# Kernel tuning notes

Measured on AMD Instinct MI355X. Metric: run time of the kernel, lower is better.

The kernel has to match this reference:

```python
import jax, jax.numpy as jnp
import numpy as np

N, E, B, D, H, C = 50000, 800000, 128, 64, 128, 2
EPS = 1e-5


def setup_inputs() -> dict:
    key = jax.random.key(0)
    ks = jax.random.split(key, 12)
    s = 0.1
    return {
        "x": jax.random.normal(ks[0], (N, D), jnp.float32),
        "edge_index": jax.random.randint(ks[1], (2, E), 0, N, jnp.int64),
        "batch": jnp.sort(jax.random.randint(ks[2], (N,), 0, B, jnp.int64)),
        "W_l": jax.random.normal(ks[3], (D, D), jnp.float32) * s,
        "b_l": jnp.zeros((D,), jnp.float32),
        "W_r": jax.random.normal(ks[4], (D, D), jnp.float32) * s,
        "W_res": jax.random.normal(ks[5], (D, D), jnp.float32) * s,
        "b_res": jnp.zeros((D,), jnp.float32),
        "gamma": jnp.ones((D,), jnp.float32),
        "beta": jnp.zeros((D,), jnp.float32),
        "gate_W1": jax.random.normal(ks[6], (D, D), jnp.float32) * s,
        "gate_b1": jnp.zeros((D,), jnp.float32),
        "gate_W2": jax.random.normal(ks[7], (D, 1), jnp.float32) * s,
        "gate_b2": jnp.zeros((1,), jnp.float32),
        "W_p1": jax.random.normal(ks[8], (D, H), jnp.float32) * s,
        "b_p1": jnp.zeros((H,), jnp.float32),
        "W_p2": jax.random.normal(ks[9], (H, C), jnp.float32) * s,
        "b_p2": jnp.zeros((C,), jnp.float32),
    }


def reference(x, edge_index, batch, W_l, b_l, W_r, W_res, b_res, gamma, beta,
              gate_W1, gate_b1, gate_W2, gate_b2, W_p1, b_p1, W_p2, b_p2):
    src, dst = edge_index[0], edge_index[1]
    # SAGEConv, mean aggregation: gather source feats, scatter-mean to target
    agg = jax.ops.segment_sum(x[src], dst, num_segments=N)          # [N, D]
    cnt = jax.ops.segment_sum(jnp.ones((E,), x.dtype), dst, num_segments=N)
    mean = agg / jnp.maximum(cnt, 1.0)[:, None]
    h = mean @ W_l + b_l + x @ W_r                                   # [N, D]
    # dropout is identity (eval mode)
    # BatchNorm1d (training-mode math: biased batch stats)
    mu = jnp.mean(h, axis=0)
    var = jnp.var(h, axis=0)
    h = (h - mu) * jax.lax.rsqrt(var + EPS) * gamma + beta
    # residual projection of the original features
    h = h + x @ W_res + b_res
    # GlobalAttention pooling: per-graph softmax over gate scores
    gate = jax.nn.relu(h @ gate_W1 + gate_b1) @ gate_W2 + gate_b2    # [N, 1]
    g = gate[:, 0]
    gmax = jax.ops.segment_max(g, batch, num_segments=B)
    gmax = jnp.where(jnp.isfinite(gmax), gmax, 0.0)
    e = jnp.exp(g - gmax[batch])
    z = jax.ops.segment_sum(e, batch, num_segments=B)
    alpha = e / jnp.maximum(z, 1e-16)[batch]
    pooled = jax.ops.segment_sum(alpha[:, None] * h, batch, num_segments=B)  # [B, D]
    # 2-layer predictor MLP with ReLU between
    out = jax.nn.relu(pooled @ W_p1 + b_p1) @ W_p2 + b_p2            # [B, C]
    return out
```

## Files before the change

kernel.cpp:

```cpp
#include <hip/hip_runtime.h>
#include <math.h>

#define N_NODES 50000
#define N_EDGES 800000
#define BATCHES 128
#define DIM 64
#define HID 128
#define NCLS 2
#define EPSV 1e-5f
#define MAXD 64

#define NPART 8
#define PART_SZ ((N_NODES + NPART - 1) / NPART)
#define EPB 2048
#define NCHK_E ((N_EDGES + EPB - 1) / EPB)
#define NCHUNK1 782

typedef __attribute__((ext_vector_type(8))) short bf16x8;
typedef __attribute__((ext_vector_type(4))) float f32x4;

__device__ __forceinline__ unsigned short f2bf(float f){
  unsigned u = __float_as_uint(f);
  u += 0x7FFFu + ((u >> 16) & 1u);
  return (unsigned short)(u >> 16);
}
__device__ __forceinline__ float bf2f(unsigned short h){
  return __uint_as_float(((unsigned)h) << 16);
}
__device__ __forceinline__ void split2(float f, unsigned short& hi, unsigned short& lo){
  hi = f2bf(f);
  lo = f2bf(f - bf2f(hi));
}
__device__ __forceinline__ uint4 pack8(const unsigned short* s){
  uint4 u;
  u.x = (unsigned)s[0] | ((unsigned)s[1] << 16);
  u.y = (unsigned)s[2] | ((unsigned)s[3] << 16);
  u.z = (unsigned)s[4] | ((unsigned)s[5] << 16);
  u.w = (unsigned)s[6] | ((unsigned)s[7] << 16);
  return u;
}

__global__ void k_scatter(const int* __restrict__ ei, int* __restrict__ cnt,
                          unsigned short* __restrict__ csr){
  const int p = blockIdx.x & (NPART-1);
  const int c = blockIdx.x >> 3;
  const int lo = p * PART_SZ;
  const int hi = lo + PART_SZ;
  const int e0 = c * EPB;
  const int e1 = (e0 + EPB < N_EDGES) ? e0 + EPB : N_EDGES;
  for (int i = e0 + threadIdx.x; i < e1; i += 256){
    int d = ei[N_EDGES + i];
    if (d >= lo && d < hi){
      int s = ei[i];
      int pos = atomicAdd(&cnt[d], 1);
      csr[(size_t)d*MAXD + pos] = (unsigned short)s;
    }
  }
}

__global__ void __launch_bounds__(256) k_lin1(
    const float* __restrict__ x, const unsigned short* __restrict__ csr,
    const int* __restrict__ cnt,
    const float* __restrict__ Wl, const float* __restrict__ bl,
    const float* __restrict__ Wr, float* __restrict__ hbuf,
    float* __restrict__ pstat){
  __shared__ __align__(16) short sB[2][64][136];
  __shared__ __align__(16) short sA[2][64][72];
  const int tid  = threadIdx.x;
  const int lane = tid & 63, w = tid >> 6;
  const int g    = lane >> 4, f = lane & 15;
  const int jc   = lane & 15;
  const int mrow = 16*w + jc;
  const int koff = (lane >> 4) * 8;
  const int r0   = 16*w + (lane >> 4)*4;
  const int base = blockIdx.x * 64;

  {
    const int k0 = 32 * w;
    #pragma unroll
    for (int kc = 0; kc < 4; ++kc){
      unsigned short h[8], l[8];
      #pragma unroll
      for (int i = 0; i < 8; ++i){
        int k = k0 + 8*kc + i;
        float v = (k < 64) ? Wl[k*DIM + lane] : Wr[(k-64)*DIM + lane];
        split2(v, h[i], l[i]);
      }
      *(uint4*)&sB[0][lane][k0 + 8*kc] = pack8(h);
      *(uint4*)&sB[1][lane][k0 + 8*kc] = pack8(l);
    }
  }
  __syncthreads();

  float blv[4];
  #pragma unroll
  for (int nt = 0; nt < 4; ++nt) blv[nt] = bl[nt*16 + jc];

  f32x4 acc[4] = {};
  #pragma unroll
  for (int half = 0; half < 2; ++half){
    if (half == 0){
      for (int n = 0; n < 16; ++n){
        const int node = base + 16*w + n;
        int dg = 0;
        if (node < N_NODES) dg = cnt[node];
        const size_t start = (size_t)node * MAXD;
        int e = (lane < dg) ? (int)csr[start + lane] : 0;
        float4 a4 = make_float4(0.f,0.f,0.f,0.f);
        int i = 0;
        for (; i + 16 <= dg; i += 16){
          int s0 = __shfl(e, i +      g, 64);
          int s1 = __shfl(e, i + 4  + g, 64);
          int s2 = __shfl(e, i + 8  + g, 64);
          int s3 = __shfl(e, i + 12 + g, 64);
          float4 v0 = *(const float4*)&x[(size_t)s0*DIM + f*4];
          float4 v1 = *(const float4*)&x[(size_t)s1*DIM + f*4];
          float4 v2 = *(const float4*)&x[(size_t)s2*DIM + f*4];
          float4 v3 = *(const float4*)&x[(size_t)s3*DIM + f*4];
          a4.x += v0.x + v1.x + v2.x + v3.x;
          a4.y += v0.y + v1.y + v2.y + v3.y;
          a4.z += v0.z + v1.z + v2.z + v3.z;
          a4.w += v0.w + v1.w + v2.w + v3.w;
        }
        for (; i < dg; i += 4){
          int idx = i + g;
          int srcl = (idx < dg) ? idx : (dg - 1);
          int s = __shfl(e, srcl, 64);
          if (idx < dg){
            float4 v = *(const float4*)&x[(size_t)s*DIM + f*4];
            a4.x += v.x; a4.y += v.y; a4.z += v.z; a4.w += v.w;
          }
        }
        a4.x += __shfl_xor(a4.x, 16, 64); a4.x += __shfl_xor(a4.x, 32, 64);
        a4.y += __shfl_xor(a4.y, 16, 64); a4.y += __shfl_xor(a4.y, 32, 64);
        a4.z += __shfl_xor(a4.z, 16, 64); a4.z += __shfl_xor(a4.z, 32, 64);
        a4.w += __shfl_xor(a4.w, 16, 64); a4.w += __shfl_xor(a4.w, 32, 64);
        if (g == 0){
          float inv = 1.f / fmaxf((float)dg, 1.f);
          unsigned short h[4], l[4];
          split2(a4.x*inv,h[0],l[0]); split2(a4.y*inv,h[1],l[1]);
          split2(a4.z*inv,h[2],l[2]); split2(a4.w*inv,h[3],l[3]);
          uint2 ph, pl;
          ph.x = (unsigned)h[0] | ((unsigned)h[1]<<16);
          ph.y = (unsigned)h[2] | ((unsigned)h[3]<<16);
          pl.x = (unsigned)l[0] | ((unsigned)l[1]<<16);
          pl.y = (unsigned)l[2] | ((unsigned)l[3]<<16);
          *(uint2*)&sA[0][16*w + n][f*4] = ph;
          *(uint2*)&sA[1][16*w + n][f*4] = pl;
        }
      }
    } else {
      #pragma unroll
      for (int s4 = 0; s4 < 4; ++s4){
        const int row = 16*w + s4*4 + g;
        const int node = base + row;
        float4 v = make_float4(0.f,0.f,0.f,0.f);
        if (node < N_NODES) v = *(const float4*)&x[(size_t)node*DIM + f*4];
        unsigned short h[4], l[4];
        split2(v.x,h[0],l[0]); split2(v.y,h[1],l[1]);
        split2(v.z,h[2],l[2]); split2(v.w,h[3],l[3]);
        uint2 ph, pl;
        ph.x = (unsigned)h[0] | ((unsigned)h[1]<<16);
        ph.y = (unsigned)h[2] | ((unsigned)h[3]<<16);
        pl.x = (unsigned)l[0] | ((unsigned)l[1]<<16);
        pl.y = (unsigned)l[2] | ((unsigned)l[3]<<16);
        *(uint2*)&sA[0][row][f*4] = ph;
        *(uint2*)&sA[1][row][f*4] = pl;
      }
    }
    #pragma unroll
    for (int kt2 = 0; kt2 < 2; ++kt2){
      const int ka = kt2*32 + koff;
      const int kb = half*64 + ka;
      bf16x8 ah = *(const bf16x8*)&sA[0][mrow][ka];
      bf16x8 al = *(const bf16x8*)&sA[1][mrow][ka];
      #pragma unroll
      for (int nt = 0; nt < 4; ++nt){
        const int nr = nt*16 + jc;
        bf16x8 bh = *(const bf16x8*)&sB[0][nr][kb];
        bf16x8 bo = *(const bf16x8*)&sB[1][nr][kb];
        acc[nt] = __builtin_amdgcn_mfma_f32_16x16x32_bf16(ah, bh, acc[nt], 0,0,0);
        acc[nt] = __builtin_amdgcn_mfma_f32_16x16x32_bf16(al, bh, acc[nt], 0,0,0);
        acc[nt] = __builtin_amdgcn_mfma_f32_16x16x32_bf16(ah, bo, acc[nt], 0,0,0);
      }
    }
  }

  float s1[4] = {0.f,0.f,0.f,0.f}, s2[4] = {0.f,0.f,0.f,0.f};
  #pragma unroll
  for (int nt = 0; nt < 4; ++nt){
    const int col = nt*16 + jc;
    #pragma unroll
    for (int r = 0; r < 4; ++r){
      const int node = base + r0 + r;
      float v = acc[nt][r] + blv[nt];
      if (node < N_NODES){
        hbuf[(size_t)node*DIM + col] = v;
        s1[nt] += v; s2[nt] += v*v;
      }
    }
  }

  __syncthreads();
  float* sred = (float*)sA;
  #pragma unroll
  for (int nt = 0; nt < 4; ++nt){
    float a = s1[nt], b = s2[nt];
    a += __shfl_xor(a, 16, 64); a += __shfl_xor(a, 32, 64);
    b += __shfl_xor(b, 16, 64); b += __shfl_xor(b, 32, 64);
    if ((lane >> 4) == 0){
      sred[0*256 + w*64 + nt*16 + jc] = a;
      sred[1*256 + w*64 + nt*16 + jc] = b;
    }
  }
  __syncthreads();
  if (tid < 64){
    float a = sred[tid] + sred[64+tid] + sred[128+tid] + sred[192+tid];
    float b = sred[256+tid] + sred[320+tid] + sred[384+tid] + sred[448+tid];
    pstat[(size_t)blockIdx.x*128 + tid]      = a;
    pstat[(size_t)blockIdx.x*128 + 64 + tid] = b;
  }
}

__global__ void __launch_bounds__(256) k_stats(
    const float* __restrict__ pstat, float* __restrict__ muinv){
  __shared__ float r1[256], r2[256];
  const int j = blockIdx.x;
  const int t = threadIdx.x;
  float s1 = 0.f, s2 = 0.f;
  for (int c = t; c < NCHUNK1; c += 256){
    s1 += pstat[(size_t)c*128 + j];
    s2 += pstat[(size_t)c*128 + 64 + j];
  }
  r1[t] = s1; r2[t] = s2;
  __syncthreads();
  for (int st = 128; st > 0; st >>= 1){
    if (t < st){ r1[t] += r1[t+st]; r2[t] += r2[t+st]; }
    __syncthreads();
  }
  if (t == 0){
    float mu = r1[0] / (float)N_NODES;
    float var = r2[0] / (float)N_NODES - mu*mu;
    muinv[j] = mu;
    muinv[DIM+j] = 1.0f / sqrtf(var + EPSV);
  }
}

__device__ __forceinline__ void stage_w64(short* sWh, short* sWl_,
                                          const float* __restrict__ W,
                                          int w, int lane){
  const int k0 = 16 * w;
  #pragma unroll
  for (int kc = 0; kc < 2; ++kc){
    unsigned short h[8], l[8];
    #pragma unroll
    for (int i = 0; i < 8; ++i){
      int k = k0 + 8*kc + i;
      split2(W[k*DIM + lane], h[i], l[i]);
    }
    *(uint4*)&sWh[lane*72 + k0 + 8*kc] = pack8(h);
    *(uint4*)&sWl_[lane*72 + k0 + 8*kc] = pack8(l);
  }
}

__global__ void __launch_bounds__(256) k_lin2(
    const float* __restrict__ x, const float* __restrict__ hbuf,
    const float* __restrict__ Wres, const float* __restrict__ bres,
    const float* __restrict__ gamma, const float* __restrict__ beta,
    const float* __restrict__ muinv,
    const float* __restrict__ gW1, const float* __restrict__ gb1,
    const float* __restrict__ gW2, const float* __restrict__ gb2,
    const int* __restrict__ batch,
    float* __restrict__ zbuf, float* __restrict__ pooled){
  __shared__ __align__(16) short sW[2][64][72];
  __shared__ __align__(16) short sA[2][64][72];
  __shared__ int sb[64];
  __shared__ unsigned long long runmask;
  const int tid  = threadIdx.x;
  const int lane = tid & 63, w = tid >> 6;
  const int jc   = lane & 15;
  const int g16  = w*4 + (lane >> 4);
  const int mrow = 16*w + jc;
  const int koff = (lane >> 4) * 8;
  const int r0   = 16*w + (lane >> 4)*4;
  const int base = blockIdx.x * 64;

  float muv[4], invv[4], gav[4], bev[4], brv[4], g1v[4], w2v[4];
  #pragma unroll
  for (int nt = 0; nt < 4; ++nt){
    const int col = nt*16 + jc;
    muv[nt] = muinv[col];  invv[nt] = muinv[DIM+col];
    gav[nt] = gamma[col];  bev[nt]  = beta[col];
    brv[nt] = bres[col];   g1v[nt]  = gb1[col];
    w2v[nt] = gW2[col];
  }
  const float gb2v = gb2[0];

  {
    const int row = tid >> 2;
    const int kq  = (tid & 3) * 16;
    const int node = base + row;
    #pragma unroll
    for (int cc = 0; cc < 4; ++cc){
      float4 v = make_float4(0.f,0.f,0.f,0.f);
      if (node < N_NODES) v = *(const float4*)&x[(size_t)node*DIM + kq + 4*cc];
      unsigned short h[4], l[4];
      split2(v.x,h[0],l[0]); split2(v.y,h[1],l[1]);
      split2(v.z,h[2],l[2]); split2(v.w,h[3],l[3]);
      uint2 ph, pl;
      ph.x = (unsigned)h[0] | ((unsigned)h[1]<<16);
      ph.y = (unsigned)h[2] | ((unsigned)h[3]<<16);
      pl.x = (unsigned)l[0] | ((unsigned)l[1]<<16);
      pl.y = (unsigned)l[2] | ((unsigned)l[3]<<16);
      *(uint2*)&sA[0][row][kq + 4*cc] = ph;
      *(uint2*)&sA[1][row][kq + 4*cc] = pl;
    }
  }
  if (tid < 64){
    int nn = base + tid;
    sb[tid] = batch[(nn < N_NODES) ? nn : (N_NODES-1)];
  }
  stage_w64(&sW[0][0][0], &sW[1][0][0], Wres, w, lane);
  __syncthreads();

  if (w == 0){
    bool fl = (lane > 0) && (sb[lane] != sb[lane-1]);
    unsigned long long mm = __ballot(fl);
    if (lane == 0) runmask = mm;
  }

  f32x4 acc[4] = {};
  #pragma unroll
  for (int kt2 = 0; kt2 < 2; ++kt2){
    const int ka = kt2*32 + koff;
    bf16x8 ah = *(const bf16x8*)&sA[0][mrow][ka];
    bf16x8 al = *(const bf16x8*)&sA[1][mrow][ka];
    #pragma unroll
    for (int nt = 0; nt < 4; ++nt){
      const int nr = nt*16 + jc;
      bf16x8 bh = *(const bf16x8*)&sW[0][nr][ka];
      bf16x8 bo = *(const bf16x8*)&sW[1][nr][ka];
      acc[nt] = __builtin_amdgcn_mfma_f32_16x16x32_bf16(ah, bh, acc[nt], 0,0,0);
      acc[nt] = __builtin_amdgcn_mfma_f32_16x16x32_bf16(al, bh, acc[nt], 0,0,0);
      acc[nt] = __builtin_amdgcn_mfma_f32_16x16x32_bf16(ah, bo, acc[nt], 0,0,0);
    }
  }

  float vk[4][4];
  #pragma unroll
  for (int nt = 0; nt < 4; ++nt){
    const int col = nt*16 + jc;
    #pragma unroll
    for (int r = 0; r < 4; ++r){
      const int node = base + r0 + r;
      float hp = 0.f;
      if (node < N_NODES) hp = hbuf[(size_t)node*DIM + col];
      float v = (hp - muv[nt])*invv[nt]*gav[nt] + bev[nt] + brv[nt] + acc[nt][r];
      vk[nt][r] = v;
      unsigned short hh, ll;
      split2(v, hh, ll);
      sA[0][r0 + r][col] = (short)hh;
      sA[1][r0 + r][col] = (short)ll;
    }
  }
  __syncthreads();
  stage_w64(&sW[0][0][0], &sW[1][0][0], gW1, w, lane);
  __syncthreads();

  f32x4 acc2[4] = {};
  #pragma unroll
  for (int kt2 = 0; kt2 < 2; ++kt2){
    const int ka = kt2*32 + koff;
    bf16x8 ah = *(const bf16x8*)&sA[0][mrow][ka];
    bf16x8 al = *(const bf16x8*)&sA[1][mrow][ka];
    #pragma unroll
    for (int nt = 0; nt < 4; ++nt){
      const int nr = nt*16 + jc;
      bf16x8 bh = *(const bf16x8*)&sW[0][nr][ka];
      bf16x8 bo = *(const bf16x8*)&sW[1][nr][ka];
      acc2[nt] = __builtin_amdgcn_mfma_f32_16x16x32_bf16(ah, bh, acc2[nt], 0,0,0);
      acc2[nt] = __builtin_amdgcn_mfma_f32_16x16x32_bf16(al, bh, acc2[nt], 0,0,0);
      acc2[nt] = __builtin_amdgcn_mfma_f32_16x16x32_bf16(ah, bo, acc2[nt], 0,0,0);
    }
  }

  float p[4] = {0.f,0.f,0.f,0.f};
  #pragma unroll
  for (int nt = 0; nt < 4; ++nt){
    #pragma unroll
    for (int r = 0; r < 4; ++r)
      p[r] += fmaxf(acc2[nt][r] + g1v[nt], 0.f) * w2v[nt];
  }
  float ev[4];
  #pragma unroll
  for (int r = 0; r < 4; ++r){
    float t = p[r];
    t += __shfl_xor(t, 1, 64); t += __shfl_xor(t, 2, 64);
    t += __shfl_xor(t, 4, 64); t += __shfl_xor(t, 8, 64);
    const int node = base + r0 + r;
    ev[r] = (node < N_NODES) ? expf(t + gb2v) : 0.f;
  }

  float* sredp = (float*)&sW[0][0][0];
  float* szl   = sredp + 16*64;
  __syncthreads();
  const unsigned long long m = runmask;
  int rstart = 0;
  while (rstart < 64){
    const int bseg = sb[rstart];
    unsigned long long rest = (rstart >= 63) ? 0ull : (m >> (rstart+1));
    const int rend = rest ? (rstart + 1 + __builtin_ctzll(rest)) : 64;
    float pacc[4] = {0.f,0.f,0.f,0.f};
    float zacc = 0.f;
    #pragma unroll
    for (int r = 0; r < 4; ++r){
      const int ln = 4*g16 + r;
      if (ln >= rstart && ln < rend){
        #pragma unroll
        for (int nt = 0; nt < 4; ++nt) pacc[nt] += ev[r]*vk[nt][r];
        zacc += ev[r];
      }
    }
    #pragma unroll
    for (int nt = 0; nt < 4; ++nt) sredp[g16*64 + nt*16 + jc] = pacc[nt];
    if ((lane & 15) == 0) szl[g16] = zacc;
    __syncthreads();
    if (tid < 64){
      float s = 0.f;
      #pragma unroll 4
      for (int g2 = 0; g2 < 16; ++g2) s += sredp[g2*64 + tid];
      atomicAdd(&pooled[bseg*DIM + tid], s);
    }
    if (tid == 64){
      float sz2 = 0.f;
      for (int g2 = 0; g2 < 16; ++g2) sz2 += szl[g2];
      atomicAdd(&zbuf[bseg], sz2);
    }
    __syncthreads();
    rstart = rend;
  }
}

__global__ void k_head(const float* __restrict__ pooled, const float* __restrict__ zbuf,
                       const float* __restrict__ Wp1, const float* __restrict__ bp1,
                       const float* __restrict__ Wp2, const float* __restrict__ bp2,
                       float* __restrict__ out){
  __shared__ float ps[DIM];
  __shared__ float red[4];
  int b = blockIdx.x;
  int t = threadIdx.x;
  if (t < DIM){
    float zz = fmaxf(zbuf[b], 1e-16f);
    ps[t] = pooled[b*DIM + t] / zz;
  }
  __syncthreads();
  float acc = bp1[t];
  #pragma unroll
  for (int d2=0; d2<DIM; d2++) acc = fmaf(ps[d2], Wp1[d2*HID + t], acc);
  acc = fmaxf(acc, 0.f);
  float o0 = acc * Wp2[t*NCLS+0];
  float o1 = acc * Wp2[t*NCLS+1];
  #pragma unroll
  for (int o=32;o>0;o>>=1){ o0 += __shfl_down(o0,o,64); o1 += __shfl_down(o1,o,64); }
  int w = t>>6;
  if ((t&63)==0){ red[w*2+0]=o0; red[w*2+1]=o1; }
  __syncthreads();
  if (t==0){
    out[b*NCLS+0] = red[0]+red[2]+bp2[0];
    out[b*NCLS+1] = red[1]+red[3]+bp2[1];
  }
}

extern "C" void kernel_launch(void* const* d_in, const int* in_sizes, int n_in,
                              void* d_out, int out_size, void* d_ws, size_t ws_size,
                              hipStream_t stream){
  const float* x     = (const float*)d_in[0];
  const int*   ei    = (const int*)d_in[1];
  const int*   batch = (const int*)d_in[2];
  const float* Wl    = (const float*)d_in[3];
  const float* bl    = (const float*)d_in[4];
  const float* Wr    = (const float*)d_in[5];
  const float* Wres  = (const float*)d_in[6];
  const float* bres  = (const float*)d_in[7];
  const float* gamma = (const float*)d_in[8];
  const float* beta  = (const float*)d_in[9];
  const float* gW1   = (const float*)d_in[10];
  const float* gb1   = (const float*)d_in[11];
  const float* gW2   = (const float*)d_in[12];
  const float* gb2   = (const float*)d_in[13];
  const float* Wp1   = (const float*)d_in[14];
  const float* bp1   = (const float*)d_in[15];
  const float* Wp2   = (const float*)d_in[16];
  const float* bp2   = (const float*)d_in[17];
  float* outp = (float*)d_out;

  int*   cnt   = (int*)d_ws;
  float* zbuf  = (float*)(cnt + N_NODES);
  float* pooled= zbuf + BATCHES;
  float* pstat = pooled + (size_t)BATCHES*DIM;
  float* muinv = pstat + (size_t)NCHUNK1*128;
  float* hbuf  = muinv + 2*DIM;
  unsigned short* csr = (unsigned short*)(hbuf + (size_t)N_NODES*DIM);

  const size_t zcount = (size_t)N_NODES + BATCHES + (size_t)BATCHES*DIM;
  hipMemsetAsync(d_ws, 0, zcount*sizeof(int), stream);

  k_scatter<<<NPART*NCHK_E, 256, 0, stream>>>(ei, cnt, csr);
  k_lin1   <<<NCHUNK1, 256, 0, stream>>>(x, csr, cnt, Wl, bl, Wr, hbuf, pstat);
  k_stats  <<<64, 256, 0, stream>>>(pstat, muinv);
  k_lin2   <<<NCHUNK1, 256, 0, stream>>>(x, hbuf, Wres, bres, gamma, beta, muinv,
                                         gW1, gb1, gW2, gb2, batch, zbuf, pooled);
  k_head   <<<BATCHES, HID, 0, stream>>>(pooled, zbuf, Wp1, bp1, Wp2, bp2, outp);
}
```

Baseline: 231.1 us.

## Split neighbor mean aggregation into separate one-wave-per-node kernel

Moves the gather-and-mean over CSR neighbors out of the fused linear kernel into a new kernel with 12,500 blocks, one wavefront per node, which writes mean features to a global buffer. The linear kernel then loads both the mean and x tiles densely. The aim is more parallelism and latency hiding for the irregular gather, which previously ran serially over 16 nodes per wave in only 782 blocks. The cost is an extra 12.8 MB write and read of the mean buffer, plus an additional kernel launch.

```diff
diff --git a/kernel.cpp b/kernel.cpp
--- a/kernel.cpp
+++ b/kernel.cpp
@@ -58,9 +58,53 @@
   }
 }
 
+__global__ void k_mean(const float* __restrict__ x,
+                       const unsigned short* __restrict__ csr,
+                       const int* __restrict__ cnt, float* __restrict__ meanb){
+  const int node = (blockIdx.x*256 + threadIdx.x) >> 6;
+  const int lane = threadIdx.x & 63;
+  const int g = lane >> 4, f = lane & 15;
+  const int dg = cnt[node];
+  const size_t start = (size_t)node * MAXD;
+  float4 acc = make_float4(0.f,0.f,0.f,0.f);
+  int e = (lane < dg) ? (int)csr[start + lane] : 0;
+  int i = 0;
+  for (; i + 16 <= dg; i += 16){
+    int s0 = __shfl(e, i +      g, 64);
+    int s1 = __shfl(e, i + 4  + g, 64);
+    int s2 = __shfl(e, i + 8  + g, 64);
+    int s3 = __shfl(e, i + 12 + g, 64);
+    float4 v0 = *(const float4*)&x[(size_t)s0*DIM + f*4];
+    float4 v1 = *(const float4*)&x[(size_t)s1*DIM + f*4];
+    float4 v2 = *(const float4*)&x[(size_t)s2*DIM + f*4];
+    float4 v3 = *(const float4*)&x[(size_t)s3*DIM + f*4];
+    acc.x += v0.x + v1.x + v2.x + v3.x;
+    acc.y += v0.y + v1.y + v2.y + v3.y;
+    acc.z += v0.z + v1.z + v2.z + v3.z;
+    acc.w += v0.w + v1.w + v2.w + v3.w;
+  }
+  for (; i < dg; i += 4){
+    int idx = i + g;
+    int srcl = (idx < dg) ? idx : (dg - 1);
+    int s = __shfl(e, srcl, 64);
+    if (idx < dg){
+      float4 v = *(const float4*)&x[(size_t)s*DIM + f*4];
+      acc.x += v.x; acc.y += v.y; acc.z += v.z; acc.w += v.w;
+    }
+  }
+  acc.x += __shfl_xor(acc.x, 16, 64); acc.x += __shfl_xor(acc.x, 32, 64);
+  acc.y += __shfl_xor(acc.y, 16, 64); acc.y += __shfl_xor(acc.y, 32, 64);
+  acc.z += __shfl_xor(acc.z, 16, 64); acc.z += __shfl_xor(acc.z, 32, 64);
+  acc.w += __shfl_xor(acc.w, 16, 64); acc.w += __shfl_xor(acc.w, 32, 64);
+  if (g == 0){
+    float inv = 1.f / fmaxf((float)dg, 1.f);
+    float4 r = make_float4(acc.x*inv, acc.y*inv, acc.z*inv, acc.w*inv);
+    *(float4*)&meanb[(size_t)node*DIM + f*4] = r;
+  }
+}
+
 __global__ void __launch_bounds__(256) k_lin1(
-    const float* __restrict__ x, const unsigned short* __restrict__ csr,
-    const int* __restrict__ cnt,
+    const float* __restrict__ meanb, const float* __restrict__ x,
     const float* __restrict__ Wl, const float* __restrict__ bl,
     const float* __restrict__ Wr, float* __restrict__ hbuf,
     float* __restrict__ pstat){
@@ -68,7 +112,6 @@
   __shared__ __align__(16) short sA[2][64][72];
   const int tid  = threadIdx.x;
   const int lane = tid & 63, w = tid >> 6;
-  const int g    = lane >> 4, f = lane & 15;
   const int jc   = lane & 15;
   const int mrow = 16*w + jc;
   const int koff = (lane >> 4) * 8;
@@ -90,7 +133,6 @@
       *(uint4*)&sB[1][lane][k0 + 8*kc] = pack8(l);
     }
   }
-  __syncthreads();
 
   float blv[4];
   #pragma unroll
@@ -99,63 +141,16 @@
   f32x4 acc[4] = {};
   #pragma unroll
   for (int half = 0; half < 2; ++half){
-    if (half == 0){
-      for (int n = 0; n < 16; ++n){
-        const int node = base + 16*w + n;
-        int dg = 0;
-        if (node < N_NODES) dg = cnt[node];
-        const size_t start = (size_t)node * MAXD;
-        int e = (lane < dg) ? (int)csr[start + lane] : 0;
-        float4 a4 = make_float4(0.f,0.f,0.f,0.f);
-        int i = 0;
-        for (; i + 16 <= dg; i += 16){
-          int s0 = __shfl(e, i +      g, 64);
-          int s1 = __shfl(e, i + 4  + g, 64);
-          int s2 = __shfl(e, i + 8  + g, 64);
-          int s3 = __shfl(e, i + 12 + g, 64);
-          float4 v0 = *(const float4*)&x[(size_t)s0*DIM + f*4];
-          float4 v1 = *(const float4*)&x[(size_t)s1*DIM + f*4];
-          float4 v2 = *(const float4*)&x[(size_t)s2*DIM + f*4];
-          float4 v3 = *(const float4*)&x[(size_t)s3*DIM + f*4];
-          a4.x += v0.x + v1.x + v2.x + v3.x;
-          a4.y += v0.y + v1.y + v2.y + v3.y;
-          a4.z += v0.z + v1.z + v2.z + v3.z;
-          a4.w += v0.w + v1.w + v2.w + v3.w;
-        }
-        for (; i < dg; i += 4){
-          int idx = i + g;
-          int srcl = (idx < dg) ? idx : (dg - 1);
-          int s = __shfl(e, srcl, 64);
-          if (idx < dg){
-            float4 v = *(const float4*)&x[(size_t)s*DIM + f*4];
-            a4.x += v.x; a4.y += v.y; a4.z += v.z; a4.w += v.w;
-          }
-        }
-        a4.x += __shfl_xor(a4.x, 16, 64); a4.x += __shfl_xor(a4.x, 32, 64);
-        a4.y += __shfl_xor(a4.y, 16, 64); a4.y += __shfl_xor(a4.y, 32, 64);
-        a4.z += __shfl_xor(a4.z, 16, 64); a4.z += __shfl_xor(a4.z, 32, 64);
-        a4.w += __shfl_xor(a4.w, 16, 64); a4.w += __shfl_xor(a4.w, 32, 64);
-        if (g == 0){
-          float inv = 1.f / fmaxf((float)dg, 1.f);
-          unsigned short h[4], l[4];
-          split2(a4.x*inv,h[0],l[0]); split2(a4.y*inv,h[1],l[1]);
-          split2(a4.z*inv,h[2],l[2]); split2(a4.w*inv,h[3],l[3]);
-          uint2 ph, pl;
-          ph.x = (unsigned)h[0] | ((unsigned)h[1]<<16);
-          ph.y = (unsigned)h[2] | ((unsigned)h[3]<<16);
-          pl.x = (unsigned)l[0] | ((unsigned)l[1]<<16);
-          pl.y = (unsigned)l[2] | ((unsigned)l[3]<<16);
-          *(uint2*)&sA[0][16*w + n][f*4] = ph;
-          *(uint2*)&sA[1][16*w + n][f*4] = pl;
-        }
-      }
-    } else {
+    const float* __restrict__ src = half ? x : meanb;
+    __syncthreads();
+    {
+      const int row = tid >> 2;
+      const int kq  = (tid & 3) * 16;
+      const int node = base + row;
       #pragma unroll
-      for (int s4 = 0; s4 < 4; ++s4){
-        const int row = 16*w + s4*4 + g;
-        const int node = base + row;
+      for (int cc = 0; cc < 4; ++cc){
         float4 v = make_float4(0.f,0.f,0.f,0.f);
-        if (node < N_NODES) v = *(const float4*)&x[(size_t)node*DIM + f*4];
+        if (node < N_NODES) v = *(const float4*)&src[(size_t)node*DIM + kq + 4*cc];
         unsigned short h[4], l[4];
         split2(v.x,h[0],l[0]); split2(v.y,h[1],l[1]);
         split2(v.z,h[2],l[2]); split2(v.w,h[3],l[3]);
@@ -164,10 +159,11 @@
         ph.y = (unsigned)h[2] | ((unsigned)h[3]<<16);
         pl.x = (unsigned)l[0] | ((unsigned)l[1]<<16);
         pl.y = (unsigned)l[2] | ((unsigned)l[3]<<16);
-        *(uint2*)&sA[0][row][f*4] = ph;
-        *(uint2*)&sA[1][row][f*4] = pl;
+        *(uint2*)&sA[0][row][kq + 4*cc] = ph;
+        *(uint2*)&sA[1][row][kq + 4*cc] = pl;
       }
     }
+    __syncthreads();
     #pragma unroll
     for (int kt2 = 0; kt2 < 2; ++kt2){
       const int ka = kt2*32 + koff;
@@ -499,14 +495,16 @@
   float* pooled= zbuf + BATCHES;
   float* pstat = pooled + (size_t)BATCHES*DIM;
   float* muinv = pstat + (size_t)NCHUNK1*128;
-  float* hbuf  = muinv + 2*DIM;
+  float* meanb = muinv + 2*DIM;
+  float* hbuf  = meanb + (size_t)N_NODES*DIM;
   unsigned short* csr = (unsigned short*)(hbuf + (size_t)N_NODES*DIM);
 
   const size_t zcount = (size_t)N_NODES + BATCHES + (size_t)BATCHES*DIM;
   hipMemsetAsync(d_ws, 0, zcount*sizeof(int), stream);
 
   k_scatter<<<NPART*NCHK_E, 256, 0, stream>>>(ei, cnt, csr);
-  k_lin1   <<<NCHUNK1, 256, 0, stream>>>(x, csr, cnt, Wl, bl, Wr, hbuf, pstat);
+  k_mean   <<<N_NODES/4, 256, 0, stream>>>(x, csr, cnt, meanb);
+  k_lin1   <<<NCHUNK1, 256, 0, stream>>>(meanb, x, Wl, bl, Wr, hbuf, pstat);
   k_stats  <<<64, 256, 0, stream>>>(pstat, muinv);
   k_lin2   <<<NCHUNK1, 256, 0, stream>>>(x, hbuf, Wres, bres, gamma, beta, muinv,
                                          gW1, gb1, gW2, gb2, batch, zbuf, pooled);
```

New measurement: 199.0 us. 13.9% less time.
